# Kernel tuning notes

Hardware: AMD Instinct MI355X
Metric: run time of the kernel (lower is better)

The kernel has to match this reference:

```python
import jax, jax.numpy as jnp
import numpy as np

B, T, D, H, L, E, K, FF, V = 2, 1024, 1024, 16, 3, 8, 2, 4096, 32000
HD = D // H


def _rmsnorm(x):
    return x * jax.lax.rsqrt(jnp.mean(x * x, axis=-1, keepdims=True) + 1e-5)


def _forward(idx, wte, wpe, wq, wk, wv, wo, gate, f1, f2, lm_head):
    Bc, Tc = idx.shape
    x = wte[idx] + wpe[:Tc]            # (B,T,D)
    x = _rmsnorm(x)
    causal = jnp.tril(jnp.ones((Tc, Tc), dtype=bool))
    total_aux = jnp.zeros((), dtype=x.dtype)
    scale = 1.0 / np.sqrt(HD)
    for l in range(L):
        xr = x
        xn = _rmsnorm(x)
        q = (xn @ wq[l].T).reshape(Bc, Tc, H, HD).transpose(0, 2, 1, 3)
        k = (xn @ wk[l].T).reshape(Bc, Tc, H, HD).transpose(0, 2, 1, 3)
        v = (xn @ wv[l].T).reshape(Bc, Tc, H, HD).transpose(0, 2, 1, 3)
        att = jnp.einsum('bhqd,bhkd->bhqk', q, k) * scale
        att = jnp.where(causal, att, -jnp.inf)
        att = jax.nn.softmax(att, axis=-1)
        o = jnp.einsum('bhqk,bhkd->bhqd', att, v)
        o = o.transpose(0, 2, 1, 3).reshape(Bc, Tc, D)
        x = o @ wo[l].T + xr
        # MoE FFN (dense compute over all experts, gather top-k)
        xr = x
        xn = _rmsnorm(x)
        gate_probs = jax.nn.softmax(jnp.einsum('btd,ed->bte', xn, gate[l]), axis=-1)
        topk_vals, topk_idx = jax.lax.top_k(gate_probs, K)   # (B,T,K)
        topk_w = topk_vals / topk_vals.sum(axis=-1, keepdims=True)
        h = jax.nn.relu(jnp.einsum('btd,efd->btef', xn, f1[l]))  # (B,T,E,FF)
        expert_stack = jnp.einsum('btef,edf->bted', h, f2[l])    # (B,T,E,D)
        selected = jnp.take_along_axis(expert_stack, topk_idx[..., None], axis=2)  # (B,T,K,D)
        moe_out = (selected * topk_w[..., None]).sum(axis=2)
        frac = gate_probs.mean(axis=(0, 1))
        total_aux = total_aux + E * jnp.sum(frac * frac)
        x = moe_out + xr
    logits = x @ lm_head.T              # (B,T,V)
    aux_loss = 0.01 * total_aux / L
    return logits, aux_loss


def setup_inputs() -> dict:
    key = jax.random.key(0)
    ks = jax.random.split(key, 12)
    s = 0.02
    return {
        'idx': jax.random.randint(ks[0], (B, T), 0, V, dtype=jnp.int64) if jax.config.jax_enable_x64 else jax.random.randint(ks[0], (B, T), 0, V, dtype=jnp.int32),
        'wte': jax.random.normal(ks[1], (V, D), jnp.float32) * s,
        'wpe': jax.random.normal(ks[2], (T, D), jnp.float32) * s,
        'wq': jax.random.normal(ks[3], (L, D, D), jnp.float32) * s,
        'wk': jax.random.normal(ks[4], (L, D, D), jnp.float32) * s,
        'wv': jax.random.normal(ks[5], (L, D, D), jnp.float32) * s,
        'wo': jax.random.normal(ks[6], (L, D, D), jnp.float32) * s,
        'gate': jax.random.normal(ks[7], (L, E, D), jnp.float32) * s,
        'f1': jax.random.normal(ks[8], (L, E, FF, D), jnp.float32) * s,
        'f2': jax.random.normal(ks[9], (L, E, D, FF), jnp.float32) * s,
        'lm_head': jax.random.normal(ks[10], (V, D), jnp.float32) * s,
    }


def reference(idx, wte, wpe, wq, wk, wv, wo, gate, f1, f2, lm_head):
    return _forward(idx, wte, wpe, wq, wk, wv, wo, gate, f1, f2, lm_head)
```

## Files before the change

### kernel.cpp

```cpp
#include <hip/hip_runtime.h>

typedef unsigned short u16;
typedef __attribute__((ext_vector_type(4))) float f32x4;
typedef __attribute__((ext_vector_type(8))) __bf16 bf16x8;
typedef __attribute__((ext_vector_type(8))) _Float16 f16x8;
typedef __attribute__((ext_vector_type(4))) unsigned short u16x4;
typedef __attribute__((ext_vector_type(8))) unsigned short u16x8;

constexpr int kT = 1024, kD = 1024, kH = 16, kHD = 64, kL = 3, kE = 8;
constexpr int kFF = 4096, kV = 32000, kBT = 2048, kSLOTS = 5120;

__device__ __forceinline__ u16 f2bf(float f) {
  union { float f; unsigned u; } v; v.f = f;
  unsigned r = v.u + 0x7FFFu + ((v.u >> 16) & 1u);
  return (u16)(r >> 16);
}
__device__ __forceinline__ u16 f2h(float x) {
  _Float16 h = (_Float16)x;
  union { _Float16 h; u16 u; } v; v.h = h; return v.u;
}
__device__ __forceinline__ void split2s(float x, u16& h, u16& m) {
  float xs = x * 64.0f;
  _Float16 hh = (_Float16)xs;
  union { _Float16 h; u16 u; } v; v.h = hh; h = v.u;
  float r = xs - (float)hh;
  union { _Float16 h; u16 u; } w; w.h = (_Float16)r; m = w.u;
}

__device__ __forceinline__ void ld_lds16(const void* g, void* l) {
  __builtin_amdgcn_global_load_lds((const __attribute__((address_space(1))) void*)g,
                                   (__attribute__((address_space(3))) void*)l, 16, 0, 0);
}

#define MFMA16(a, b, c) __builtin_amdgcn_mfma_f32_16x16x32_bf16(a, b, c, 0, 0, 0)
#define MFMAH(a, b, c)  __builtin_amdgcn_mfma_f32_16x16x32_f16(a, b, c, 0, 0, 0)

__device__ __forceinline__ float blockReduceSum256(float v) {
  #pragma unroll
  for (int m = 32; m >= 1; m >>= 1) v += __shfl_xor(v, m);
  __shared__ float sh_[4];
  int w = threadIdx.x >> 6;
  if ((threadIdx.x & 63) == 0) sh_[w] = v;
  __syncthreads();
  v = (sh_[0] + sh_[1]) + (sh_[2] + sh_[3]);
  __syncthreads();
  return v;
}


__global__ __launch_bounds__(256) void cast_bf16_k(const float* __restrict__ in,
                                                   u16* __restrict__ out, long n4) {
  long i = (long)blockIdx.x * 256 + threadIdx.x;
  long stride = (long)gridDim.x * 256;
  for (; i < n4; i += stride) {
    f32x4 v = ((const f32x4*)in)[i];
    u16x4 o; o[0] = f2bf(v[0]); o[1] = f2bf(v[1]); o[2] = f2bf(v[2]); o[3] = f2bf(v[3]);
    ((u16x4*)out)[i] = o;
  }
}

__global__ __launch_bounds__(256) void cast_h_k(const float* __restrict__ in,
                                                u16* __restrict__ out, long n4) {
  long i = (long)blockIdx.x * 256 + threadIdx.x;
  long stride = (long)gridDim.x * 256;
  for (; i < n4; i += stride) {
    f32x4 v = ((const f32x4*)in)[i];
    u16x4 o; o[0] = f2h(v[0]); o[1] = f2h(v[1]); o[2] = f2h(v[2]); o[3] = f2h(v[3]);
    ((u16x4*)out)[i] = o;
  }
}

__global__ __launch_bounds__(256) void qkvcomb_k(const float* __restrict__ a,
    const float* __restrict__ b, u16* __restrict__ oP, long plane, long n4) {
  long i = (long)blockIdx.x * 256 + threadIdx.x;
  long stride = (long)gridDim.x * 256;
  for (; i < n4; i += stride) {
    f32x4 v = ((const f32x4*)a)[i] + ((const f32x4*)b)[i];
    u16x4 hh, mm;
    #pragma unroll
    for (int j = 0; j < 4; ++j) {
      u16 h, m; split2s(v[j], h, m);
      hh[j] = h; mm[j] = m;
    }
    ((u16x4*)oP)[i] = hh;
    ((u16x4*)(oP + plane))[i] = mm;
  }
}

__global__ __launch_bounds__(256) void embed_rms_k(const int* __restrict__ idx,
    const float* __restrict__ wte, const float* __restrict__ wpe, float* __restrict__ x) {
  int tok = blockIdx.x, t = threadIdx.x;
  int id = idx[tok];
  int tt = tok & (kT - 1);
  f32x4 a = ((const f32x4*)(wte + (long)id * kD))[t];
  f32x4 p = ((const f32x4*)(wpe + (long)tt * kD))[t];
  f32x4 vv = a + p;
  float ss = vv[0]*vv[0] + vv[1]*vv[1] + vv[2]*vv[2] + vv[3]*vv[3];
  ss = blockReduceSum256(ss);
  float sc = rsqrtf(ss * (1.0f / kD) + 1e-5f);
  vv *= sc;
  ((f32x4*)(x + (long)tok * kD))[t] = vv;
}

__global__ __launch_bounds__(256) void rmsnorm2_k(const float* __restrict__ x,
    float* __restrict__ xnf, u16* __restrict__ xnb) {
  int tok = blockIdx.x, t = threadIdx.x;
  f32x4 vv = ((const f32x4*)(x + (long)tok * kD))[t];
  float ss = blockReduceSum256(vv[0]*vv[0] + vv[1]*vv[1] + vv[2]*vv[2] + vv[3]*vv[3]);
  float sc = rsqrtf(ss * (1.0f / kD) + 1e-5f);
  vv *= sc;
  ((f32x4*)(xnf + (long)tok * kD))[t] = vv;
  u16x4 o;
  o[0] = f2bf(vv[0]); o[1] = f2bf(vv[1]); o[2] = f2bf(vv[2]); o[3] = f2bf(vv[3]);
  ((u16x4*)(xnb + (long)tok * kD))[t] = o;
}

__global__ __launch_bounds__(256) void rmsnorm2h_k(const float* __restrict__ x,
    u16* __restrict__ xnP, long plane) {
  int tok = blockIdx.x, t = threadIdx.x;
  f32x4 vv = ((const f32x4*)(x + (long)tok * kD))[t];
  float ss = blockReduceSum256(vv[0]*vv[0] + vv[1]*vv[1] + vv[2]*vv[2] + vv[3]*vv[3]);
  float sc = rsqrtf(ss * (1.0f / kD) + 1e-5f);
  vv *= sc;
  u16x4 a, b;
  #pragma unroll
  for (int j = 0; j < 4; ++j) {
    u16 h, m; split2s(vv[j], h, m);
    a[j] = h; b[j] = m;
  }
  long o = (long)tok * kD / 4 + t;
  ((u16x4*)xnP)[o] = a;
  ((u16x4*)(xnP + plane))[o] = b;
}

__global__ __launch_bounds__(256) void resid4_rms2h_k(float* __restrict__ x,
    const float* __restrict__ parts, long plane, u16* __restrict__ xnP, long xplane) {
  int tok = blockIdx.x, t = threadIdx.x;
  long o = (long)tok * (kD / 4) + t;
  f32x4 xv = ((f32x4*)x)[o];
  #pragma unroll
  for (int p = 0; p < 4; ++p) xv += ((const f32x4*)(parts + p * plane))[o];
  ((f32x4*)x)[o] = xv;
  float ss = blockReduceSum256(xv[0]*xv[0] + xv[1]*xv[1] + xv[2]*xv[2] + xv[3]*xv[3]);
  float sc = rsqrtf(ss * (1.0f / kD) + 1e-5f);
  f32x4 vv = xv * sc;
  u16x4 a, b;
  #pragma unroll
  for (int j = 0; j < 4; ++j) {
    u16 h, m; split2s(vv[j], h, m);
    a[j] = h; b[j] = m;
  }
  ((u16x4*)xnP)[o] = a;
  ((u16x4*)(xnP + xplane))[o] = b;
}

__global__ __launch_bounds__(256) void moe4_rms2h_k(float* __restrict__ x,
    const float* __restrict__ outsP, long plane, const int* __restrict__ slotOf,
    const float* __restrict__ top2w, u16* __restrict__ xnP, long xplane) {
  int tok = blockIdx.x, t = threadIdx.x;
  int s0 = slotOf[tok*2], s1 = slotOf[tok*2+1];
  float w0 = top2w[tok*2], w1 = top2w[tok*2+1];
  f32x4 a = {0.f,0.f,0.f,0.f}, b = a;
  #pragma unroll
  for (int p = 0; p < 4; ++p) {
    a += ((const f32x4*)(outsP + p * plane + (long)s0 * kD))[t];
    b += ((const f32x4*)(outsP + p * plane + (long)s1 * kD))[t];
  }
  long o = (long)tok * (kD / 4) + t;
  f32x4 xv = ((f32x4*)x)[o];
  xv += a * w0 + b * w1;
  ((f32x4*)x)[o] = xv;
  float ss = blockReduceSum256(xv[0]*xv[0] + xv[1]*xv[1] + xv[2]*xv[2] + xv[3]*xv[3]);
  float sc = rsqrtf(ss * (1.0f / kD) + 1e-5f);
  f32x4 vv = xv * sc;
  u16x4 ha, hb;
  #pragma unroll
  for (int j = 0; j < 4; ++j) {
    u16 h, m; split2s(vv[j], h, m);
    ha[j] = h; hb[j] = m;
  }
  ((u16x4*)xnP)[o] = ha;
  ((u16x4*)(xnP + xplane))[o] = hb;
}

__global__ __launch_bounds__(256) void moe4_cast_h_k(float* __restrict__ x,
    const float* __restrict__ outsP, long plane, const int* __restrict__ slotOf,
    const float* __restrict__ top2w, u16* __restrict__ xn) {
  int tok = blockIdx.x, t = threadIdx.x;
  int s0 = slotOf[tok*2], s1 = slotOf[tok*2+1];
  float w0 = top2w[tok*2], w1 = top2w[tok*2+1];
  f32x4 a = {0.f,0.f,0.f,0.f}, b = a;
  #pragma unroll
  for (int p = 0; p < 4; ++p) {
    a += ((const f32x4*)(outsP + p * plane + (long)s0 * kD))[t];
    b += ((const f32x4*)(outsP + p * plane + (long)s1 * kD))[t];
  }
  long o = (long)tok * (kD / 4) + t;
  f32x4 xv = ((f32x4*)x)[o];
  xv += a * w0 + b * w1;
  u16x4 hv;
  #pragma unroll
  for (int j = 0; j < 4; ++j) hv[j] = f2h(xv[j]);
  ((u16x4*)xn)[o] = hv;
}

__global__ __launch_bounds__(256) void gate_topk_k(const float* __restrict__ x,
    const float* __restrict__ gate_l, float* __restrict__ probs, int* __restrict__ top2e,
    float* __restrict__ top2w, int* __restrict__ counts) {
  int tok = blockIdx.x, t = threadIdx.x;
  f32x4 xv = ((const f32x4*)(x + (long)tok * kD))[t];
  float ss = blockReduceSum256(xv[0]*xv[0] + xv[1]*xv[1] + xv[2]*xv[2] + xv[3]*xv[3]);
  float sc = rsqrtf(ss * (1.0f / kD) + 1e-5f);
  float a[kE];
  #pragma unroll
  for (int e = 0; e < kE; ++e) {
    f32x4 gv = ((const f32x4*)(gate_l + (long)e * kD))[t];
    a[e] = xv[0]*gv[0] + xv[1]*gv[1] + xv[2]*gv[2] + xv[3]*gv[3];
  }
  __shared__ float sh8[kE][4];
  int w = t >> 6, l = t & 63;
  #pragma unroll
  for (int e = 0; e < kE; ++e) {
    float v = a[e];
    #pragma unroll
    for (int m = 32; m >= 1; m >>= 1) v += __shfl_xor(v, m);
    if (l == 0) sh8[e][w] = v;
  }
  __syncthreads();
  if (t == 0) {
    float lg[kE], mx = -1e30f;
    #pragma unroll
    for (int e = 0; e < kE; ++e) {
      lg[e] = (sh8[e][0] + sh8[e][1] + sh8[e][2] + sh8[e][3]) * sc;
      mx = fmaxf(mx, lg[e]);
    }
    float pe[kE], s = 0.f;
    #pragma unroll
    for (int e = 0; e < kE; ++e) { pe[e] = __expf(lg[e] - mx); s += pe[e]; }
    float inv = 1.f / s;
    int i1 = 0;
    #pragma unroll
    for (int e = 1; e < kE; ++e) if (lg[e] > lg[i1]) i1 = e;
    int i2 = (i1 == 0) ? 1 : 0;
    #pragma unroll
    for (int e = 0; e < kE; ++e) if (e != i1 && lg[e] > lg[i2]) i2 = e;
    #pragma unroll
    for (int e = 0; e < kE; ++e) probs[(long)tok * kE + e] = pe[e] * inv;
    float p1 = pe[i1] * inv, p2 = pe[i2] * inv;
    float wn = p1 + p2;
    top2e[tok*2] = i1; top2e[tok*2+1] = i2;
    top2w[tok*2] = p1 / wn; top2w[tok*2+1] = p2 / wn;
    atomicAdd(&counts[i1], 1); atomicAdd(&counts[i2], 1);
  }
}

__global__ void calc_offsets_k(const int* __restrict__ counts, int* __restrict__ offsets) {
  if (threadIdx.x == 0) {
    int o = 0;
    #pragma unroll
    for (int e = 0; e < kE; ++e) { offsets[e] = o; o += (counts[e] + 127) & ~127; }
    offsets[kE] = o;
  }
}

__global__ __launch_bounds__(256) void fill_slots2_k(const int* __restrict__ top2e,
    const int* __restrict__ counts, int* __restrict__ offsets, int* __restrict__ cursors,
    int* __restrict__ rows, int* __restrict__ slotOf) {
  __shared__ int soff[kE + 1];
  if (threadIdx.x == 0) {
    int o = 0;
    #pragma unroll
    for (int e = 0; e < kE; ++e) { soff[e] = o; o += (counts[e] + 127) & ~127; }
    soff[kE] = o;
    if (blockIdx.x == 0) {
      #pragma unroll
      for (int e = 0; e <= kE; ++e) offsets[e] = soff[e];
    }
  }
  __syncthreads();
  int tok = blockIdx.x * 256 + threadIdx.x;
  if (tok >= kBT) return;
  #pragma unroll
  for (int j = 0; j < 2; ++j) {
    int e = top2e[tok*2 + j];
    int pos = atomicAdd(&cursors[e], 1);
    int slot = soff[e] + pos;
    rows[slot] = tok;
    slotOf[tok*2 + j] = slot;
  }
}

__global__ __launch_bounds__(256) void moe_combine4_k(float* __restrict__ x,
    const float* __restrict__ outsP, long plane, const int* __restrict__ slotOf,
    const float* __restrict__ top2w) {
  int tok = blockIdx.x, t = threadIdx.x;
  int s0 = slotOf[tok*2], s1 = slotOf[tok*2+1];
  float w0 = top2w[tok*2], w1 = top2w[tok*2+1];
  f32x4 a = {0.f,0.f,0.f,0.f}, b = a;
  #pragma unroll
  for (int p = 0; p < 4; ++p) {
    a += ((const f32x4*)(outsP + p * plane + (long)s0 * kD))[t];
    b += ((const f32x4*)(outsP + p * plane + (long)s1 * kD))[t];
  }
  f32x4 xv = ((f32x4*)(x + (long)tok * kD))[t];
  xv += a * w0 + b * w1;
  ((f32x4*)(x + (long)tok * kD))[t] = xv;
}

__global__ __launch_bounds__(256) void aux_reduce3_k(const float* __restrict__ probs3,
    long plane, float* __restrict__ outv) {
  int t = threadIdx.x;
  float part[kL][kE] = {};
  for (int i = t; i < kBT; i += 256) {
    #pragma unroll
    for (int l = 0; l < kL; ++l)
      #pragma unroll
      for (int e = 0; e < kE; ++e)
        part[l][e] += probs3[l * plane + (long)i * kE + e];
  }
  __shared__ float sh[kL][kE][4];
  int w = t >> 6, ln = t & 63;
  #pragma unroll
  for (int l = 0; l < kL; ++l)
    #pragma unroll
    for (int e = 0; e < kE; ++e) {
      float v = part[l][e];
      #pragma unroll
      for (int m = 32; m >= 1; m >>= 1) v += __shfl_xor(v, m);
      if (ln == 0) sh[l][e][w] = v;
    }
  __syncthreads();
  if (t == 0) {
    float acc = 0.f;
    #pragma unroll
    for (int l = 0; l < kL; ++l)
      #pragma unroll
      for (int e = 0; e < kE; ++e) {
        float frac = (sh[l][e][0] + sh[l][e][1] + sh[l][e][2] + sh[l][e][3]) * (1.0f / kBT);
        acc += frac * frac;
      }
    outv[0] = 0.01f * (float)kE * acc / (float)kL;
  }
}

__global__ __launch_bounds__(256) void aux_reduce_k(const float* __restrict__ probs,
                                                    float* __restrict__ aux) {
  int t = threadIdx.x;
  float part[kE] = {};
  for (int i = t; i < kBT; i += 256) {
    #pragma unroll
    for (int e = 0; e < kE; ++e) part[e] += probs[(long)i * kE + e];
  }
  __shared__ float sh8[kE][4];
  int w = t >> 6, l = t & 63;
  #pragma unroll
  for (int e = 0; e < kE; ++e) {
    float v = part[e];
    #pragma unroll
    for (int m = 32; m >= 1; m >>= 1) v += __shfl_xor(v, m);
    if (l == 0) sh8[e][w] = v;
  }
  __syncthreads();
  if (t == 0) {
    float acc = 0.f;
    #pragma unroll
    for (int e = 0; e < kE; ++e) {
      float frac = (sh8[e][0] + sh8[e][1] + sh8[e][2] + sh8[e][3]) * (1.0f / kBT);
      acc += frac * frac;
    }
    aux[0] += (float)kE * acc;
  }
}

__global__ void write_aux_k(const float* __restrict__ aux, float* __restrict__ out) {
  if (threadIdx.x == 0) out[0] = 0.01f * aux[0] / (float)kL;
}

enum { P_BF16 = 0, P_BF16_RELU = 1, P_F32 = 2, P_F32_RESID = 3, P_F32_RELU = 4,
       P_SPLIT2_RELU = 5, P_F16_RELU = 6 };

__device__ __forceinline__ int clamp_row(int rv) {
  return ((unsigned)rv < (unsigned)kBT) ? rv : 0;
}

template <bool MPART>
__device__ __forceinline__ void block_mn(int lin, int base, int mArg, int& mb, int& nb) {
  int xcd = lin & 7, c = lin >> 3;
  if (MPART) {
    mb = xcd * mArg + (c % mArg);
    nb = c / mArg;
  } else {
    int swz = xcd * (base >> 3) + c;
    mb = swz % mArg;
    nb = swz / mArg;
  }
}


template <int POST, bool GATHER, bool EXPERT, bool MPART, bool BF32, bool QKV3 = false>
__global__ __launch_bounds__(256) void gemm2h_bt_k(
    const u16* __restrict__ A0, long planeA,
    const void* __restrict__ Bv, const void* __restrict__ Bv1, const void* __restrict__ Bv2,
    long planeB,
    void* __restrict__ C, long planeC,
    const float* __restrict__ resid,
    const int* __restrict__ rows, const int* __restrict__ offsets,
    int N, int K, int lda, long eBstride, int mArg,
    int kParts, int base, long cPart) {
  constexpr int BM = 128, BK = 32;
  int part = blockIdx.x / base;
  int lin = blockIdx.x % base;
  int mb, nb;
  block_mn<MPART>(lin, base, mArg, mb, nb);
  int m0 = mb * BM, n0 = nb * BM;
  const u16* B0 = (const u16*)Bv;
  const float* Bf = (const float*)Bv;
  if (EXPERT) {
    int total = offsets[kE];
    if (m0 >= total) return;
    int e = 0;
    while (offsets[e + 1] <= m0) ++e;
    if (BF32) Bf += (long)e * eBstride; else B0 += (long)e * eBstride;
  }
  __shared__ __align__(16) u16 Ac[BM][64];
  __shared__ __align__(16) u16 Bc[BM][64];
  int t = threadIdx.x;
  int l = t & 63, lr = l & 15, lg = l >> 4;
  int wid = t >> 6;
  int wm = (wid >> 1) * 64, wn = (wid & 1) * 64;

  long asrc[4], bsrc[4];
  int ldst[4];
  #pragma unroll
  for (int it = 0; it < 4; ++it) {
    int d = it * 256 + t;
    int row = d >> 3, pc = d & 7;
    int lc = pc ^ (row & 7);
    int p = lc >> 2, c = lc & 3;
    int grow = GATHER ? clamp_row(rows[m0 + row]) : (m0 + row);
    asrc[it] = (long)p * planeA + (long)grow * lda + c * 8;
    if (!BF32) bsrc[it] = (long)p * planeB + (long)(n0 + row) * K + c * 8;
    ldst[it] = (it * 256 + (t & ~63)) * 8;
  }
  long bsrcF[2];
  int brow[2], bc[2];
  if (BF32) {
    if (QKV3) {
      int ts = n0 >> 10;
      Bf = (ts == 0) ? (const float*)Bv : (ts == 1) ? (const float*)Bv1
                                                    : (const float*)Bv2;
    }
    int nB = QKV3 ? (n0 & 1023) : n0;
    #pragma unroll
    for (int it = 0; it < 2; ++it) {
      int d = it * 256 + t;
      brow[it] = d >> 2; bc[it] = d & 3;
      bsrcF[it] = (long)(nB + brow[it]) * K + bc[it] * 8;
    }
  }
  int sa = lr & 7;
  int cH = (lg ^ sa) * 8;
  int cM = ((4 + lg) ^ sa) * 8;

  f32x4 acc[4][4];
  #pragma unroll
  for (int i = 0; i < 4; ++i)
    #pragma unroll
    for (int j = 0; j < 4; ++j) acc[i][j] = 0.f;

  int kStep = K / kParts;
  int kLo = part * kStep, kHi = kLo + kStep;

  f32x4 pv0[2], pv1[2];
  if (BF32) {
    #pragma unroll
    for (int it = 0; it < 2; ++it) {
      const float* src = Bf + bsrcF[it] + kLo;
      pv0[it] = *(const f32x4*)src;
      pv1[it] = *(const f32x4*)(src + 4);
    }
  }
  for (int k0 = kLo; k0 < kHi; k0 += BK) {
    bool pf = BF32 && (k0 + BK < kHi);
    #pragma unroll
    for (int it = 0; it < 4; ++it) {
      ld_lds16(A0 + asrc[it] + k0, &Ac[0][0] + ldst[it]);
      if (!BF32) ld_lds16(B0 + bsrc[it] + k0, &Bc[0][0] + ldst[it]);
    }
    f32x4 nv0[2], nv1[2];
    if (pf) {
      #pragma unroll
      for (int it = 0; it < 2; ++it) {
        const float* src = Bf + bsrcF[it] + k0 + BK;
        nv0[it] = *(const f32x4*)src;
        nv1[it] = *(const f32x4*)(src + 4);
      }
    }
    if (BF32) {
      #pragma unroll
      for (int it = 0; it < 2; ++it) {
        u16x8 hi, mi;
        #pragma unroll
        for (int j = 0; j < 4; ++j) {
          u16 h, m; split2s(pv0[it][j], h, m); hi[j] = h; mi[j] = m;
        }
        #pragma unroll
        for (int j = 0; j < 4; ++j) {
          u16 h, m; split2s(pv1[it][j], h, m); hi[4 + j] = h; mi[4 + j] = m;
        }
        int r7 = brow[it] & 7;
        *(u16x8*)&Bc[brow[it]][(bc[it] ^ r7) * 8] = hi;
        *(u16x8*)&Bc[brow[it]][((4 + bc[it]) ^ r7) * 8] = mi;
      }
    }
    __syncthreads();
    f16x8 ah[4], am[4];
    #pragma unroll
    for (int i = 0; i < 4; ++i) {
      ah[i] = *(const f16x8*)&Ac[wm + i*16 + lr][cH];
      am[i] = *(const f16x8*)&Ac[wm + i*16 + lr][cM];
    }
    __builtin_amdgcn_s_setprio(1);
    #pragma unroll
    for (int j = 0; j < 4; ++j) {
      f16x8 bh = *(const f16x8*)&Bc[wn + j*16 + lr][cH];
      f16x8 bm = *(const f16x8*)&Bc[wn + j*16 + lr][cM];
      #pragma unroll
      for (int i = 0; i < 4; ++i) {
        acc[i][j] = MFMAH(ah[i], bh, acc[i][j]);
        acc[i][j] = MFMAH(am[i], bh, acc[i][j]);
        acc[i][j] = MFMAH(ah[i], bm, acc[i][j]);
      }
    }
    __builtin_amdgcn_s_setprio(0);
    __syncthreads();
    if (pf) {
      #pragma unroll
      for (int it = 0; it < 2; ++it) { pv0[it] = nv0[it]; pv1[it] = nv1[it]; }
    }
  }
  float* Cf = (float*)C + (long)part * cPart;
  #pragma unroll
  for (int i = 0; i < 4; ++i) {
    #pragma unroll
    for (int r = 0; r < 4; ++r) {
      long m = m0 + wm + i*16 + lg*4 + r;
      #pragma unroll
      for (int j = 0; j < 4; ++j) {
        int n = n0 + wn + j*16 + lr;
        float val = acc[i][j][r] * (1.0f / 4096.0f);
        if (POST == P_F32) {
          Cf[m * N + n] = val;
        } else if (POST == P_F32_RESID) {
          ((float*)C)[m * N + n] = val + resid[m * N + n];
        } else if (POST == P_SPLIT2_RELU) {
          val = fmaxf(val, 0.f);
          u16 h, mm; split2s(val, h, mm);
          u16* Cp = (u16*)C;
          Cp[m * N + n] = h;
          Cp[planeC + m * N + n] = mm;
        }
      }
    }
  }
}


template <int POST, bool GATHER, bool EXPERT, bool BF32>
__global__ __launch_bounds__(512) void gemm2hW_bt_k(
    const u16* __restrict__ A0, long planeA,
    const void* __restrict__ Bv, long planeB,
    void* __restrict__ C, long planeC,
    const int* __restrict__ rows, const int* __restrict__ offsets,
    int N, int K, int lda, long eBstride, int mPerX,
    int kParts, int base, long cPart) {
  constexpr int BM = 128, BN = 256, BK = 32;
  int part = blockIdx.x / base;
  int lin = blockIdx.x % base;
  int xcd = lin & 7, c0 = lin >> 3;
  int m0 = (xcd * mPerX + (c0 % mPerX)) * BM;
  int n0 = (c0 / mPerX) * BN;
  const u16* B0 = (const u16*)Bv;
  const float* Bf = (const float*)Bv;
  if (EXPERT) {
    int total = offsets[kE];
    if (m0 >= total) return;
    int e = 0;
    while (offsets[e + 1] <= m0) ++e;
    if (BF32) Bf += (long)e * eBstride; else B0 += (long)e * eBstride;
  }
  __shared__ __align__(16) u16 Ac[BM][64];
  __shared__ __align__(16) u16 Bc[BN][64];
  int t = threadIdx.x;
  int l = t & 63, lr = l & 15, lg = l >> 4;
  int wid = t >> 6;
  int wm = (wid >> 2) * 64;
  int wn = (wid & 3) * 64;

  long asrc[2], bsrc[4];
  int aldst[2], bldst[4];
  #pragma unroll
  for (int it = 0; it < 2; ++it) {
    int d = it * 512 + t;
    int row = d >> 3, pc = d & 7;
    int lc = pc ^ (row & 7);
    int p = lc >> 2, cc = lc & 3;
    int grow = GATHER ? clamp_row(rows[m0 + row]) : (m0 + row);
    asrc[it] = (long)p * planeA + (long)grow * lda + cc * 8;
    aldst[it] = (it * 512 + (t & ~63)) * 8;
  }
  long bsrcF[2];
  int brow[2], bcc[2];
  if (!BF32) {
    #pragma unroll
    for (int it = 0; it < 4; ++it) {
      int d = it * 512 + t;
      int row = d >> 3, pc = d & 7;
      int lc = pc ^ (row & 7);
      int p = lc >> 2, cc = lc & 3;
      bsrc[it] = (long)p * planeB + (long)(n0 + row) * K + cc * 8;
      bldst[it] = (it * 512 + (t & ~63)) * 8;
    }
  } else {
    #pragma unroll
    for (int it = 0; it < 2; ++it) {
      int d = it * 512 + t;
      brow[it] = d >> 2; bcc[it] = d & 3;
      bsrcF[it] = (long)(n0 + brow[it]) * K + bcc[it] * 8;
    }
  }
  int sa = lr & 7;
  int cH = (lg ^ sa) * 8;
  int cM = ((4 + lg) ^ sa) * 8;

  f32x4 acc[4][4];
  #pragma unroll
  for (int i = 0; i < 4; ++i)
    #pragma unroll
    for (int j = 0; j < 4; ++j) acc[i][j] = 0.f;

  int kStep = K / kParts;
  int kLo = part * kStep, kHi = kLo + kStep;

  f32x4 pv0[2], pv1[2];
  if (BF32) {
    #pragma unroll
    for (int it = 0; it < 2; ++it) {
      const float* src = Bf + bsrcF[it] + kLo;
      pv0[it] = *(const f32x4*)src;
      pv1[it] = *(const f32x4*)(src + 4);
    }
  }
  for (int k0 = kLo; k0 < kHi; k0 += BK) {
    bool pf = BF32 && (k0 + BK < kHi);
    #pragma unroll
    for (int it = 0; it < 2; ++it)
      ld_lds16(A0 + asrc[it] + k0, &Ac[0][0] + aldst[it]);
    if (!BF32) {
      #pragma unroll
      for (int it = 0; it < 4; ++it)
        ld_lds16(B0 + bsrc[it] + k0, &Bc[0][0] + bldst[it]);
    }
    f32x4 nv0[2], nv1[2];
    if (pf) {
      #pragma unroll
      for (int it = 0; it < 2; ++it) {
        const float* src = Bf + bsrcF[it] + k0 + BK;
        nv0[it] = *(const f32x4*)src;
        nv1[it] = *(const f32x4*)(src + 4);
      }
    }
    if (BF32) {
      #pragma unroll
      for (int it = 0; it < 2; ++it) {
        u16x8 hi, mi;
        #pragma unroll
        for (int j = 0; j < 4; ++j) {
          u16 h, m; split2s(pv0[it][j], h, m); hi[j] = h; mi[j] = m;
        }
        #pragma unroll
        for (int j = 0; j < 4; ++j) {
          u16 h, m; split2s(pv1[it][j], h, m); hi[4 + j] = h; mi[4 + j] = m;
        }
        int r7 = brow[it] & 7;
        *(u16x8*)&Bc[brow[it]][(bcc[it] ^ r7) * 8] = hi;
        *(u16x8*)&Bc[brow[it]][((4 + bcc[it]) ^ r7) * 8] = mi;
      }
    }
    __syncthreads();
    f16x8 ah[4], am[4];
    #pragma unroll
    for (int i = 0; i < 4; ++i) {
      ah[i] = *(const f16x8*)&Ac[wm + i*16 + lr][cH];
      am[i] = *(const f16x8*)&Ac[wm + i*16 + lr][cM];
    }
    __builtin_amdgcn_s_setprio(1);
    #pragma unroll
    for (int j = 0; j < 4; ++j) {
      f16x8 bh = *(const f16x8*)&Bc[wn + j*16 + lr][cH];
      f16x8 bm = *(const f16x8*)&Bc[wn + j*16 + lr][cM];
      #pragma unroll
      for (int i = 0; i < 4; ++i) {
        acc[i][j] = MFMAH(ah[i], bh, acc[i][j]);
        acc[i][j] = MFMAH(am[i], bh, acc[i][j]);
        acc[i][j] = MFMAH(ah[i], bm, acc[i][j]);
      }
    }
    __builtin_amdgcn_s_setprio(0);
    __syncthreads();
    if (pf) {
      #pragma unroll
      for (int it = 0; it < 2; ++it) { pv0[it] = nv0[it]; pv1[it] = nv1[it]; }
    }
  }
  float* Cf = (float*)C + (long)part * cPart;
  #pragma unroll
  for (int i = 0; i < 4; ++i) {
    #pragma unroll
    for (int r = 0; r < 4; ++r) {
      long m = m0 + wm + i*16 + lg*4 + r;
      #pragma unroll
      for (int j = 0; j < 4; ++j) {
        int n = n0 + wn + j*16 + lr;
        float val = acc[i][j][r] * (1.0f / 4096.0f);
        if (POST == P_F32) {
          Cf[m * N + n] = val;
        } else if (POST == P_SPLIT2_RELU) {
          val = fmaxf(val, 0.f);
          u16 h, mm; split2s(val, h, mm);
          u16* Cp = (u16*)C;
          Cp[m * N + n] = h;
          Cp[planeC + m * N + n] = mm;
        }
      }
    }
  }
}


template <int POST, bool EXPERT, bool GATHER, bool HALF, bool BCONV, bool MPART>
__global__ __launch_bounds__(256) void gemm_bt_k(
    const u16* __restrict__ A, const void* __restrict__ Bv, void* __restrict__ C,
    const int* __restrict__ rows, const int* __restrict__ offsets,
    int N, int K, int lda, long eBstride, float oscale, int mArg,
    int kParts, int base, long cPart) {
  constexpr int BM = 128, BK = 64;
  int part = blockIdx.x / base;
  int lin = blockIdx.x % base;
  int mb, nb;
  block_mn<MPART>(lin, base, mArg, mb, nb);
  int m0 = mb * BM, n0 = nb * BM;
  const float* Bf = (const float*)Bv;
  const u16*   Bh = (const u16*)Bv;
  if (EXPERT) {
    int total = offsets[kE];
    if (m0 >= total) return;
    int e = 0;
    while (offsets[e + 1] <= m0) ++e;
    if (BCONV) Bf += (long)e * eBstride; else Bh += (long)e * eBstride;
  }
  __shared__ __align__(16) u16 As[BM][BK];
  __shared__ __align__(16) u16 Bs[BM][BK];
  int t = threadIdx.x;
  int l = t & 63, lr = l & 15, lg = l >> 4;
  int wid = t >> 6;
  int wm = (wid >> 1) * 64, wn = (wid & 1) * 64;

  long asrc[4], bsrc[4];
  int ldst[4];
  #pragma unroll
  for (int it = 0; it < 4; ++it) {
    int d = it * 256 + t;
    int row = d >> 3, pc = d & 7;
    int c = pc ^ (row & 7);
    int grow = GATHER ? clamp_row(rows[m0 + row]) : (m0 + row);
    asrc[it] = (long)grow * lda + c * 8;
    if (!BCONV) bsrc[it] = (long)(n0 + row) * K + c * 8;
    ldst[it] = (it * 256 + (t & ~63)) * 8;
  }
  long bsrcC[4];
  int bdst[4];
  if (BCONV) {
    #pragma unroll
    for (int it = 0; it < 4; ++it) {
      int d = it * 256 + t;
      int row = d >> 3, lc = d & 7;
      bsrcC[it] = (long)(n0 + row) * K + lc * 8;
      bdst[it] = row * BK + (lc ^ (row & 7)) * 8;
    }
  }
  f32x4 acc[4][4];
  #pragma unroll
  for (int i = 0; i < 4; ++i)
    #pragma unroll
    for (int j = 0; j < 4; ++j) acc[i][j] = 0.f;

  int kStep = K / kParts;
  int kLo = part * kStep, kHi = kLo + kStep;
  for (int k0 = kLo; k0 < kHi; k0 += BK) {
    #pragma unroll
    for (int it = 0; it < 4; ++it)
      ld_lds16(A + asrc[it] + k0, &As[0][0] + ldst[it]);
    if (!BCONV) {
      #pragma unroll
      for (int it = 0; it < 4; ++it)
        ld_lds16(Bh + bsrc[it] + k0, &Bs[0][0] + ldst[it]);
    } else {
      #pragma unroll
      for (int it = 0; it < 4; ++it) {
        const float* src = Bf + bsrcC[it] + k0;
        f32x4 v0 = *(const f32x4*)src;
        f32x4 v1 = *(const f32x4*)(src + 4);
        u16x8 o;
        #pragma unroll
        for (int j = 0; j < 4; ++j) {
          o[j] = HALF ? f2h(v0[j]) : f2bf(v0[j]);
          o[4 + j] = HALF ? f2h(v1[j]) : f2bf(v1[j]);
        }
        *(u16x8*)(&Bs[0][0] + bdst[it]) = o;
      }
    }
    __syncthreads();
    __builtin_amdgcn_s_setprio(1);
    #pragma unroll
    for (int kk = 0; kk < 2; ++kk) {
      int ca = ((kk * 4 + lg) ^ (lr & 7)) * 8;
      #pragma unroll
      for (int i = 0; i < 4; ++i)
        #pragma unroll
        for (int j = 0; j < 4; ++j) {
          if (HALF) {
            f16x8 af = *(const f16x8*)&As[wm + i*16 + lr][ca];
            f16x8 bq = *(const f16x8*)&Bs[wn + j*16 + lr][ca];
            acc[i][j] = MFMAH(af, bq, acc[i][j]);
          } else {
            bf16x8 af = *(const bf16x8*)&As[wm + i*16 + lr][ca];
            bf16x8 bq = *(const bf16x8*)&Bs[wn + j*16 + lr][ca];
            acc[i][j] = MFMA16(af, bq, acc[i][j]);
          }
        }
    }
    __builtin_amdgcn_s_setprio(0);
    __syncthreads();
  }
  #pragma unroll
  for (int i = 0; i < 4; ++i) {
    #pragma unroll
    for (int r = 0; r < 4; ++r) {
      long m = m0 + wm + i*16 + lg*4 + r;
      #pragma unroll
      for (int j = 0; j < 4; ++j) {
        int n = n0 + wn + j*16 + lr;
        float val = acc[i][j][r] * oscale;
        if (POST == P_BF16_RELU)       ((u16*)C)[m * N + n] = f2bf(fmaxf(val, 0.f));
        else if (POST == P_F16_RELU)   ((u16*)C)[m * N + n] = f2h(fmaxf(val, 0.f));
        else if (POST == P_F32)        ((float*)C + (long)part * cPart)[m * N + n] = val;
      }
    }
  }
}


template <int POST, bool GATHER, bool EXPERT>
__global__ __launch_bounds__(256) void sgemm_bt_k(
    const float* __restrict__ A, const float* __restrict__ B, float* __restrict__ C,
    const float* __restrict__ resid, const int* __restrict__ rows,
    const int* __restrict__ offsets, int N, int K, int lda, long eBstride) {
  constexpr int BM = 128, BN = 128, BK = 32;
  int m0 = blockIdx.x * BM, n0 = blockIdx.y * BN;
  if (EXPERT) {
    int total = offsets[kE];
    if (m0 >= total) return;
    int e = 0;
    while (offsets[e + 1] <= m0) ++e;
    B += (long)e * eBstride;
  }
  __shared__ float Ast[BK][BM];
  __shared__ float Bst[BK][BN];
  int t = threadIdx.x, tx = t & 15, ty = t >> 4;
  long asrc[4], bsrc[4];
  #pragma unroll
  for (int it = 0; it < 4; ++it) {
    int c = it * 256 + t;
    int row = c >> 3, kc = (c & 7) * 4;
    int gr = GATHER ? clamp_row(rows[m0 + row]) : (m0 + row);
    asrc[it] = (long)gr * lda + kc;
    bsrc[it] = (long)(n0 + row) * K + kc;
  }
  f32x4 accv[8][2];
  #pragma unroll
  for (int i = 0; i < 8; ++i) { accv[i][0] = 0.f; accv[i][1] = 0.f; }

  for (int k0 = 0; k0 < K; k0 += BK) {
    #pragma unroll
    for (int it = 0; it < 4; ++it) {
      int c = it * 256 + t;
      int row = c >> 3, kc = (c & 7) * 4;
      f32x4 av = *(const f32x4*)(A + asrc[it] + k0);
      f32x4 bv = *(const f32x4*)(B + bsrc[it] + k0);
      #pragma unroll
      for (int j = 0; j < 4; ++j) { Ast[kc + j][row] = av[j]; Bst[kc + j][row] = bv[j]; }
    }
    __syncthreads();
    #pragma unroll
    for (int kk = 0; kk < BK; ++kk) {
      f32x4 a0 = *(const f32x4*)&Ast[kk][ty * 4];
      f32x4 a1 = *(const f32x4*)&Ast[kk][64 + ty * 4];
      f32x4 b0 = *(const f32x4*)&Bst[kk][tx * 4];
      f32x4 b1 = *(const f32x4*)&Bst[kk][64 + tx * 4];
      float as[8] = {a0[0], a0[1], a0[2], a0[3], a1[0], a1[1], a1[2], a1[3]};
      #pragma unroll
      for (int i = 0; i < 8; ++i) {
        accv[i][0] += b0 * as[i];
        accv[i][1] += b1 * as[i];
      }
    }
    __syncthreads();
  }
  #pragma unroll
  for (int ih = 0; ih < 2; ++ih)
    #pragma unroll
    for (int i = 0; i < 4; ++i) {
      long m = m0 + ih * 64 + ty * 4 + i;
      #pragma unroll
      for (int jh = 0; jh < 2; ++jh) {
        long n = n0 + jh * 64 + tx * 4;
        f32x4 val = accv[ih * 4 + i][jh];
        if (POST == P_F32_RELU) {
          #pragma unroll
          for (int j = 0; j < 4; ++j) val[j] = fmaxf(val[j], 0.f);
        }
        if (POST == P_F32_RESID) val += *(const f32x4*)&resid[m * N + n];
        *(f32x4*)&C[m * N + n] = val;
      }
    }
}


__global__ __launch_bounds__(256) void attn2h_k(
    const u16* __restrict__ qkvP, long qplane,
    u16* __restrict__ oP, long oplane) {
  int qt = (int)gridDim.x - 1 - (int)blockIdx.x;
  int bh = blockIdx.y;
  int b = bh >> 4, h = bh & 15;
  const int ldq = 3 * kD;
  long hbq = (long)b * kT * ldq + h * kHD;
  long hbo = (long)b * kT * kD + h * kHD;
  int t = threadIdx.x, w = t >> 6, l = t & 63;
  int lr = l & 15, lg = l >> 4;

  __shared__ __align__(16) u16 Ks[2][64][72];
  __shared__ __align__(16) u16 Vt[2][64][72];
  __shared__ __align__(16) u16 Ps[2][4][16][72];

  f16x8 qf0[2], qf1[2];
  {
    long qrow = qt * 64 + w * 16 + lr;
    const u16* qp = qkvP + hbq + qrow * ldq;
    #pragma unroll
    for (int kc = 0; kc < 2; ++kc) {
      qf0[kc] = *(const f16x8*)(qp + kc * 32 + lg * 8);
      qf1[kc] = *(const f16x8*)(qp + qplane + kc * 32 + lg * 8);
    }
  }
  int qg = qt * 64 + w * 16 + lg * 4;

  float mrow[4], lsum[4];
  f32x4 accO[4];
  #pragma unroll
  for (int r = 0; r < 4; ++r) { mrow[r] = -1e30f; lsum[r] = 0.f; }
  #pragma unroll
  for (int j = 0; j < 4; ++j) accO[j] = 0.f;

  for (int it = 0; it <= qt; ++it) {
    #pragma unroll
    for (int p = 0; p < 2; ++p) {
      #pragma unroll
      for (int s = 0; s < 2; ++s) {
        int c = s * 256 + t;
        int row = c >> 3, col = (c & 7) * 8;
        long gi = (long)p * qplane + hbq + (long)(it * 64 + row) * ldq + col;
        *(u16x8*)&Ks[p][row][col] = *(const u16x8*)(qkvP + kD + gi);
        u16x8 vv = *(const u16x8*)(qkvP + 2 * kD + gi);
        #pragma unroll
        for (int j = 0; j < 8; ++j) Vt[p][col + j][row] = vv[j];
      }
    }
    __syncthreads();

    f32x4 s4[4];
    __builtin_amdgcn_s_setprio(1);
    #pragma unroll
    for (int j = 0; j < 4; ++j) {
      f32x4 z = {0.f, 0.f, 0.f, 0.f};
      #pragma unroll
      for (int kc = 0; kc < 2; ++kc) {
        f16x8 kh = *(const f16x8*)&Ks[0][j*16 + lr][kc*32 + lg*8];
        f16x8 km = *(const f16x8*)&Ks[1][j*16 + lr][kc*32 + lg*8];
        z = MFMAH(qf0[kc], kh, z);
        z = MFMAH(qf1[kc], kh, z);
        z = MFMAH(qf0[kc], km, z);
      }
      s4[j] = z;
    }
    __builtin_amdgcn_s_setprio(0);
    #pragma unroll
    for (int j = 0; j < 4; ++j)
      #pragma unroll
      for (int r = 0; r < 4; ++r) {
        float sv = s4[j][r] * (0.125f / 4096.0f);
        if (it * 64 + j * 16 + lr > qg + r) sv = -1e30f;
        s4[j][r] = sv;
      }
    float alpha[4];
    #pragma unroll
    for (int r = 0; r < 4; ++r) {
      float mx = fmaxf(fmaxf(s4[0][r], s4[1][r]), fmaxf(s4[2][r], s4[3][r]));
      mx = fmaxf(mx, __shfl_xor(mx, 1));
      mx = fmaxf(mx, __shfl_xor(mx, 2));
      mx = fmaxf(mx, __shfl_xor(mx, 4));
      mx = fmaxf(mx, __shfl_xor(mx, 8));
      float mi = fmaxf(mrow[r], mx);
      alpha[r] = __expf(mrow[r] - mi);
      mrow[r] = mi;
    }
    float rs[4] = {0.f, 0.f, 0.f, 0.f};
    #pragma unroll
    for (int j = 0; j < 4; ++j)
      #pragma unroll
      for (int r = 0; r < 4; ++r) {
        float p = __expf(s4[j][r] - mrow[r]);
        rs[r] += p;
        u16 hh, mm; split2s(p, hh, mm);
        Ps[0][w][lg*4 + r][j*16 + lr] = hh;
        Ps[1][w][lg*4 + r][j*16 + lr] = mm;
      }
    #pragma unroll
    for (int r = 0; r < 4; ++r) {
      float x2 = rs[r];
      x2 += __shfl_xor(x2, 1);
      x2 += __shfl_xor(x2, 2);
      x2 += __shfl_xor(x2, 4);
      x2 += __shfl_xor(x2, 8);
      lsum[r] = lsum[r] * alpha[r] + x2;
    }
    #pragma unroll
    for (int j = 0; j < 4; ++j)
      #pragma unroll
      for (int r = 0; r < 4; ++r) accO[j][r] *= alpha[r];
    __syncthreads();

    f16x8 ph[2], pm[2];
    #pragma unroll
    for (int kc = 0; kc < 2; ++kc) {
      ph[kc] = *(const f16x8*)&Ps[0][w][lr][kc*32 + lg*8];
      pm[kc] = *(const f16x8*)&Ps[1][w][lr][kc*32 + lg*8];
    }
    __builtin_amdgcn_s_setprio(1);
    #pragma unroll
    for (int j2 = 0; j2 < 4; ++j2) {
      #pragma unroll
      for (int kc = 0; kc < 2; ++kc) {
        f16x8 vh = *(const f16x8*)&Vt[0][j2*16 + lr][kc*32 + lg*8];
        f16x8 vm = *(const f16x8*)&Vt[1][j2*16 + lr][kc*32 + lg*8];
        accO[j2] = MFMAH(ph[kc], vh, accO[j2]);
        accO[j2] = MFMAH(pm[kc], vh, accO[j2]);
        accO[j2] = MFMAH(ph[kc], vm, accO[j2]);
      }
    }
    __builtin_amdgcn_s_setprio(0);
    __syncthreads();
  }
  #pragma unroll
  for (int j2 = 0; j2 < 4; ++j2)
    #pragma unroll
    for (int r = 0; r < 4; ++r) {
      float ov = accO[j2][r] * (1.0f / 4096.0f) / lsum[r];
      long row = qt * 64 + w * 16 + lg * 4 + r;
      long idx = hbo + row * kD + j2 * 16 + lr;
      u16 hh, mm; split2s(ov, hh, mm);
      oP[idx] = hh;
      oP[oplane + idx] = mm;
    }
}


__global__ __launch_bounds__(256) void attn_f32_k(
    const float* __restrict__ qkv, float* __restrict__ of32, int ldq) {
  int qt = blockIdx.x;
  int bh = blockIdx.y;
  int b = bh >> 4, h = bh & 15;
  long hbq = (long)b * kT * ldq + h * kHD;
  long hbo = (long)b * kT * kD + h * kHD;
  int t = threadIdx.x, qr = t >> 2, sub = t & 3;

  __shared__ float Qs[64][68], Ks[64][68], Vs[64][68], Ps[64][68];

  const float* q = qkv;
  const float* k = qkv + kD;
  const float* v = qkv + 2 * kD;

  #pragma unroll
  for (int it = 0; it < 4; ++it) {
    int c = it * 256 + t, row = c >> 4, c4 = (c & 15) * 4;
    f32x4 qv = *(const f32x4*)(q + hbq + (long)(qt * 64 + row) * ldq + c4);
    #pragma unroll
    for (int j = 0; j < 4; ++j) Qs[row][c4 + j] = qv[j];
  }
  __syncthreads();
  f32x4 qreg[16];
  #pragma unroll
  for (int d4 = 0; d4 < 16; ++d4) qreg[d4] = *(const f32x4*)&Qs[qr][d4 * 4];
  int qg = qt * 64 + qr;

  float mrow = -1e30f, lsum = 0.f;
  f32x4 accO[4];
  #pragma unroll
  for (int i = 0; i < 4; ++i) accO[i] = 0.f;

  for (int itl = 0; itl <= qt; ++itl) {
    #pragma unroll
    for (int it = 0; it < 4; ++it) {
      int c = it * 256 + t, row = c >> 4, c4 = (c & 15) * 4;
      long gi = hbq + (long)(itl * 64 + row) * ldq + c4;
      f32x4 kv = *(const f32x4*)(k + gi);
      f32x4 vv = *(const f32x4*)(v + gi);
      #pragma unroll
      for (int j = 0; j < 4; ++j) { Ks[row][c4 + j] = kv[j]; Vs[row][c4 + j] = vv[j]; }
    }
    __syncthreads();

    float s[16];
    #pragma unroll
    for (int kk = 0; kk < 16; ++kk) {
      int key = kk * 4 + sub;
      f32x4 a = {0.f, 0.f, 0.f, 0.f};
      #pragma unroll
      for (int d4 = 0; d4 < 16; ++d4) a += qreg[d4] * *(const f32x4*)&Ks[key][d4 * 4];
      float sv = (a[0] + a[1] + a[2] + a[3]) * 0.125f;
      if (itl * 64 + key > qg) sv = -1e30f;
      s[kk] = sv;
    }
    float mx = s[0];
    #pragma unroll
    for (int kk = 1; kk < 16; ++kk) mx = fmaxf(mx, s[kk]);
    mx = fmaxf(mx, __shfl_xor(mx, 1));
    mx = fmaxf(mx, __shfl_xor(mx, 2));
    float mi = fmaxf(mrow, mx);
    float alpha = __expf(mrow - mi);
    mrow = mi;
    float rs = 0.f;
    #pragma unroll
    for (int kk = 0; kk < 16; ++kk) {
      float p = __expf(s[kk] - mi);
      rs += p;
      Ps[qr][kk * 4 + sub] = p;
    }
    rs += __shfl_xor(rs, 1);
    rs += __shfl_xor(rs, 2);
    lsum = lsum * alpha + rs;
    #pragma unroll
    for (int i = 0; i < 4; ++i) accO[i] *= alpha;
    #pragma unroll
    for (int key2 = 0; key2 < 64; ++key2) {
      float p = Ps[qr][key2];
      #pragma unroll
      for (int i4 = 0; i4 < 4; ++i4)
        accO[i4] += p * *(const f32x4*)&Vs[key2][sub * 16 + i4 * 4];
    }
    __syncthreads();
  }
  float inv = 1.f / lsum;
  #pragma unroll
  for (int i4 = 0; i4 < 4; ++i4) {
    f32x4 ov = accO[i4] * inv;
    *(f32x4*)(of32 + hbo + (long)qg * kD + sub * 16 + i4 * 4) = ov;
  }
}


extern "C" void kernel_launch(void* const* d_in, const int* in_sizes, int n_in,
                              void* d_out, int out_size, void* d_ws, size_t ws_size,
                              hipStream_t stream) {
  const int*   idx  = (const int*)  d_in[0];
  const float* wte  = (const float*)d_in[1];
  const float* wpe  = (const float*)d_in[2];
  const float* wq   = (const float*)d_in[3];
  const float* wk   = (const float*)d_in[4];
  const float* wv   = (const float*)d_in[5];
  const float* wo   = (const float*)d_in[6];
  const float* gate = (const float*)d_in[7];
  const float* f1   = (const float*)d_in[8];
  const float* f2   = (const float*)d_in[9];
  const float* lmh  = (const float*)d_in[10];
  float* out = (float*)d_out;

  char* ws = (char*)d_ws;
  size_t off = 0;
  auto alloc = [&](size_t b) -> char* {
    char* p = ws + off;
    off += (b + 255) & ~(size_t)255;
    return p;
  };

  constexpr long PLN_XN = (long)kBT * kD;
  constexpr long PLN_Q3 = (long)kBT * 3 * kD;
  constexpr long PLN_FF = (long)kE * kFF * kD;
  constexpr long PLN_H = (long)kSLOTS * kFF;
  constexpr long PLN_OUTS = (long)kSLOTS * kD;
  constexpr long PLN_PR = (long)kBT * kE;

  float* x     = (float*)alloc((size_t)kBT * kD * 4);
  float* outs  = (float*)alloc((size_t)4 * PLN_OUTS * 4);
  float* probs3= (float*)alloc((size_t)kL * PLN_PR * 4);
  int*   top2e = (int*)  alloc((size_t)kBT * 2 * 4);
  float* top2w = (float*)alloc((size_t)kBT * 2 * 4);
  int*   meta  = (int*)  alloc(64 * 4);
  int* counts = meta; int* cursors = meta + 8; int* offs = meta + 16;
  int*   rows  = (int*)  alloc((size_t)kSLOTS * 4);
  int*   slotOf= (int*)  alloc((size_t)kBT * 2 * 4);
  float* aux   = (float*)alloc(256);
  size_t off_shared = off;

  u16*   xnP   = (u16*)  alloc((size_t)2 * PLN_XN * 2);
  float* qkvf  = (float*)alloc((size_t)PLN_Q3 * 4);
  u16*   qkvP  = (u16*)  alloc((size_t)2 * PLN_Q3 * 2);
  u16*   ofP   = (u16*)  alloc((size_t)2 * PLN_XN * 2);
  u16*   hP    = (u16*)  alloc((size_t)2 * PLN_H * 2);
  u16*   lmb   = (u16*)  alloc((size_t)kV * kD * 2);
  bool fast = (off <= ws_size);
  float* qkvp1 = (float*)hP;

  dim3 gAttn(kT / 64, 2 * kH);
  int bQKV = (kBT / 128) * (3 * kD / 128);
  int bWO  = (kBT / 128) * (kD / 128);
  int nF1W = (kSLOTS / 128) * (kFF / 256);
  int bF2  = (kSLOTS / 128) * (kD / 128);
  int nF1s = (kSLOTS / 128) * (kFF / 128);
  int nLM  = (kBT / 128) * (kV / 128);

  if (fast) {
    cast_h_k<<<4096, 256, 0, stream>>>(lmh, lmb, (long)kV * kD / 4);
    embed_rms_k<<<kBT, 256, 0, stream>>>(idx, wte, wpe, x);
    rmsnorm2h_k<<<kBT, 256, 0, stream>>>(x, xnP, PLN_XN);

    for (int li = 0; li < kL; ++li) {
      size_t dd = (size_t)li * kD * kD;
      gemm2h_bt_k<P_F32, false, false, true, true, true><<<2 * bQKV, 256, 0, stream>>>(
          xnP, PLN_XN, wq + dd, wk + dd, wv + dd, 0,
          qkvf, 0, nullptr, nullptr, nullptr, 3 * kD, kD, kD, 0, 2,
          2, bQKV, (long)(qkvp1 - qkvf));
      qkvcomb_k<<<2048, 256, 0, stream>>>(qkvf, qkvp1, qkvP, PLN_Q3, PLN_Q3 / 4);
      attn2h_k<<<gAttn, 256, 0, stream>>>(qkvP, PLN_Q3, ofP, PLN_XN);
      gemm2h_bt_k<P_F32, false, false, true, true><<<4 * bWO, 256, 0, stream>>>(
          ofP, PLN_XN, wo + dd, nullptr, nullptr, 0,
          outs, 0, nullptr, nullptr, nullptr, kD, kD, kD, 0, 2,
          4, bWO, PLN_OUTS);
      resid4_rms2h_k<<<kBT, 256, 0, stream>>>(x, outs, PLN_OUTS, xnP, PLN_XN);
      hipMemsetAsync(meta, 0, 64, stream);
      gate_topk_k<<<kBT, 256, 0, stream>>>(x, gate + (size_t)li * kE * kD,
                                           probs3 + (size_t)li * PLN_PR,
                                           top2e, top2w, counts);
      fill_slots2_k<<<kBT / 256, 256, 0, stream>>>(top2e, counts, offs, cursors,
                                                   rows, slotOf);
      size_t fd = (size_t)li * PLN_FF;
      if (li < 2) {
        gemm2hW_bt_k<P_SPLIT2_RELU, true, true, true><<<nF1W, 512, 0, stream>>>(
            xnP, PLN_XN, f1 + fd, 0, hP, PLN_H, rows, offs,
            kFF, kD, kD, (long)kFF * kD, kSLOTS / 128 / 8,
            1, nF1W, 0);
        gemm2h_bt_k<P_F32, false, true, true, true><<<4 * bF2, 256, 0, stream>>>(
            hP, PLN_H, f2 + fd, nullptr, nullptr, 0, outs, 0, nullptr, nullptr, offs,
            kD, kFF, kFF, (long)kD * kFF, kSLOTS / 128 / 8,
            4, bF2, PLN_OUTS);
        moe4_rms2h_k<<<kBT, 256, 0, stream>>>(x, outs, PLN_OUTS, slotOf, top2w,
                                              xnP, PLN_XN);
      } else {
        gemm_bt_k<P_F16_RELU, true, true, true, true, true><<<nF1s, 256, 0, stream>>>(
            xnP, f1 + fd, hP, rows, offs, kFF, kD, kD, (long)kFF * kD,
            1.0f / 64.0f, kSLOTS / 128 / 8, 1, nF1s, 0);
        gemm_bt_k<P_F32, true, false, true, true, true><<<4 * bF2, 256, 0, stream>>>(
            hP, f2 + fd, outs, nullptr, offs, kD, kFF, kFF, (long)kD * kFF,
            1.0f, kSLOTS / 128 / 8, 4, bF2, PLN_OUTS);
        moe4_cast_h_k<<<kBT, 256, 0, stream>>>(x, outs, PLN_OUTS, slotOf, top2w, xnP);
      }
    }
    gemm_bt_k<P_F32, false, false, true, false, false><<<nLM, 256, 0, stream>>>(
        xnP, lmb, out, nullptr, nullptr, kV, kD, kD, 0, 1.0f, kBT / 128,
        1, nLM, 0);
    aux_reduce3_k<<<1, 256, 0, stream>>>(probs3, PLN_PR, out + (size_t)kBT * kV);
    return;
  }

  off = off_shared;
  float* xnf   = (float*)alloc((size_t)kBT * kD * 4);
  u16*   xnb   = (u16*)  alloc((size_t)kBT * kD * 2);
  float* qkvf32= (float*)alloc((size_t)kBT * 3 * kD * 4);
  float* off32 = (float*)alloc((size_t)kBT * kD * 4);
  float* hbuf  = (float*)alloc((size_t)kSLOTS * kFF * 4);
  u16* hbuf16 = (u16*)hbuf;

  hipMemsetAsync(aux, 0, 4, stream);
  embed_rms_k<<<kBT, 256, 0, stream>>>(idx, wte, wpe, x);
  dim3 gF1s(kSLOTS / 128, kFF / 128);
  dim3 gF2s(kSLOTS / 128, kD / 128);
  for (int li = 0; li < kL; ++li) {
    size_t dd = (size_t)li * kD * kD;
    rmsnorm2_k<<<kBT, 256, 0, stream>>>(x, xnf, xnb);
    dim3 gP(kBT / 128, kD / 128);
    sgemm_bt_k<P_F32, false, false><<<gP, 256, 0, stream>>>(
        xnf, wq + dd, qkvf32, nullptr, nullptr, nullptr, 3 * kD, kD, kD, 0);
    sgemm_bt_k<P_F32, false, false><<<gP, 256, 0, stream>>>(
        xnf, wk + dd, qkvf32 + kD, nullptr, nullptr, nullptr, 3 * kD, kD, kD, 0);
    sgemm_bt_k<P_F32, false, false><<<gP, 256, 0, stream>>>(
        xnf, wv + dd, qkvf32 + 2 * kD, nullptr, nullptr, nullptr, 3 * kD, kD, kD, 0);
    attn_f32_k<<<gAttn, 256, 0, stream>>>(qkvf32, off32, 3 * kD);
    sgemm_bt_k<P_F32_RESID, false, false><<<gP, 256, 0, stream>>>(
        off32, wo + dd, x, x, nullptr, nullptr, kD, kD, kD, 0);
    rmsnorm2_k<<<kBT, 256, 0, stream>>>(x, xnf, xnb);
    hipMemsetAsync(meta, 0, 64, stream);
    gate_topk_k<<<kBT, 256, 0, stream>>>(x, gate + (size_t)li * kE * kD,
                                         probs3, top2e, top2w, counts);
    calc_offsets_k<<<1, 64, 0, stream>>>(counts, offs);
    fill_slots2_k<<<kBT / 256, 256, 0, stream>>>(top2e, counts, offs, cursors,
                                                 rows, slotOf);
    size_t fd = (size_t)li * kE * kFF * kD;
    if (li < 2) {
      sgemm_bt_k<P_F32_RELU, true, true><<<gF1s, 256, 0, stream>>>(
          xnf, f1 + fd, hbuf, nullptr, rows, offs, kFF, kD, kD, (long)kFF * kD);
      sgemm_bt_k<P_F32, false, true><<<gF2s, 256, 0, stream>>>(
          hbuf, f2 + fd, outs, nullptr, nullptr, offs, kD, kFF, kFF, (long)kD * kFF);
    } else {
      gemm_bt_k<P_BF16_RELU, true, true, false, true, false><<<nF1s, 256, 0, stream>>>(
          xnb, f1 + fd, hbuf16, rows, offs, kFF, kD, kD, (long)kFF * kD,
          1.0f, kSLOTS / 128, 1, nF1s, 0);
      gemm_bt_k<P_F32, true, false, false, true, false><<<bF2, 256, 0, stream>>>(
          hbuf16, f2 + fd, outs, nullptr, offs, kD, kFF, kFF, (long)kD * kFF,
          1.0f, kSLOTS / 128, 1, bF2, 0);
    }
    hipMemsetAsync(outs + PLN_OUTS, 0, 3 * PLN_OUTS * 4, stream);
    moe_combine4_k<<<kBT, 256, 0, stream>>>(x, outs, PLN_OUTS, slotOf, top2w);
    aux_reduce_k<<<1, 256, 0, stream>>>(probs3, aux);
  }
  cast_bf16_k<<<2048, 256, 0, stream>>>(x, xnb, (long)kBT * kD / 4);
  gemm_bt_k<P_F32, false, false, false, true, false><<<nLM, 256, 0, stream>>>(
      xnb, lmh, out, nullptr, nullptr, kV, kD, kD, 0, 1.0f, kBT / 128,
      1, nLM, 0);
  write_aux_k<<<1, 64, 0, stream>>>(aux, out + (size_t)kBT * kV);
}
```

Baseline: 1.842 ms.

## Fuse lm_head fp16 cast into GEMM B-load and prefetch converted B tiles

Drops the standalone kernel that casts the 32000x1024 lm_head to fp16 and instead has the LM-head GEMM read fp32 weights and convert them on the fly (BCONV path). It also adds register double-buffering for the BCONV path, loading the next K-tile's fp32 B values while the current tile is converted and multiplied. This removes a full write-and-reread of the converted weight matrix, but the GEMM now reads twice the bytes for B and carries extra registers for the prefetch.

```diff
diff --git a/kernel.cpp b/kernel.cpp
--- a/kernel.cpp
+++ b/kernel.cpp
@@ -55,17 +55,6 @@
   for (; i < n4; i += stride) {
     f32x4 v = ((const f32x4*)in)[i];
     u16x4 o; o[0] = f2bf(v[0]); o[1] = f2bf(v[1]); o[2] = f2bf(v[2]); o[3] = f2bf(v[3]);
-    ((u16x4*)out)[i] = o;
-  }
-}
-
-__global__ __launch_bounds__(256) void cast_h_k(const float* __restrict__ in,
-                                                u16* __restrict__ out, long n4) {
-  long i = (long)blockIdx.x * 256 + threadIdx.x;
-  long stride = (long)gridDim.x * 256;
-  for (; i < n4; i += stride) {
-    f32x4 v = ((const f32x4*)in)[i];
-    u16x4 o; o[0] = f2h(v[0]); o[1] = f2h(v[1]); o[2] = f2h(v[2]); o[3] = f2h(v[3]);
     ((u16x4*)out)[i] = o;
   }
 }
@@ -797,7 +786,18 @@
 
   int kStep = K / kParts;
   int kLo = part * kStep, kHi = kLo + kStep;
+
+  f32x4 pv0[4], pv1[4];
+  if (BCONV) {
+    #pragma unroll
+    for (int it = 0; it < 4; ++it) {
+      const float* src = Bf + bsrcC[it] + kLo;
+      pv0[it] = *(const f32x4*)src;
+      pv1[it] = *(const f32x4*)(src + 4);
+    }
+  }
   for (int k0 = kLo; k0 < kHi; k0 += BK) {
+    bool pf = BCONV && (k0 + BK < kHi);
     #pragma unroll
     for (int it = 0; it < 4; ++it)
       ld_lds16(A + asrc[it] + k0, &As[0][0] + ldst[it]);
@@ -805,17 +805,24 @@
       #pragma unroll
       for (int it = 0; it < 4; ++it)
         ld_lds16(Bh + bsrc[it] + k0, &Bs[0][0] + ldst[it]);
-    } else {
+    }
+    f32x4 nv0[4], nv1[4];
+    if (pf) {
       #pragma unroll
       for (int it = 0; it < 4; ++it) {
-        const float* src = Bf + bsrcC[it] + k0;
-        f32x4 v0 = *(const f32x4*)src;
-        f32x4 v1 = *(const f32x4*)(src + 4);
+        const float* src = Bf + bsrcC[it] + k0 + BK;
+        nv0[it] = *(const f32x4*)src;
+        nv1[it] = *(const f32x4*)(src + 4);
+      }
+    }
+    if (BCONV) {
+      #pragma unroll
+      for (int it = 0; it < 4; ++it) {
         u16x8 o;
         #pragma unroll
         for (int j = 0; j < 4; ++j) {
-          o[j] = HALF ? f2h(v0[j]) : f2bf(v0[j]);
-          o[4 + j] = HALF ? f2h(v1[j]) : f2bf(v1[j]);
+          o[j] = HALF ? f2h(pv0[it][j]) : f2bf(pv0[it][j]);
+          o[4 + j] = HALF ? f2h(pv1[it][j]) : f2bf(pv1[it][j]);
         }
         *(u16x8*)(&Bs[0][0] + bdst[it]) = o;
       }
@@ -842,6 +849,10 @@
     }
     __builtin_amdgcn_s_setprio(0);
     __syncthreads();
+    if (pf) {
+      #pragma unroll
+      for (int it = 0; it < 4; ++it) { pv0[it] = nv0[it]; pv1[it] = nv1[it]; }
+    }
   }
   #pragma unroll
   for (int i = 0; i < 4; ++i) {
@@ -1227,7 +1238,6 @@
   u16*   qkvP  = (u16*)  alloc((size_t)2 * PLN_Q3 * 2);
   u16*   ofP   = (u16*)  alloc((size_t)2 * PLN_XN * 2);
   u16*   hP    = (u16*)  alloc((size_t)2 * PLN_H * 2);
-  u16*   lmb   = (u16*)  alloc((size_t)kV * kD * 2);
   bool fast = (off <= ws_size);
   float* qkvp1 = (float*)hP;
 
@@ -1240,7 +1250,6 @@
   int nLM  = (kBT / 128) * (kV / 128);
 
   if (fast) {
-    cast_h_k<<<4096, 256, 0, stream>>>(lmh, lmb, (long)kV * kD / 4);
     embed_rms_k<<<kBT, 256, 0, stream>>>(idx, wte, wpe, x);
     rmsnorm2h_k<<<kBT, 256, 0, stream>>>(x, xnP, PLN_XN);
 
@@ -1285,8 +1294,8 @@
         moe4_cast_h_k<<<kBT, 256, 0, stream>>>(x, outs, PLN_OUTS, slotOf, top2w, xnP);
       }
     }
-    gemm_bt_k<P_F32, false, false, true, false, false><<<nLM, 256, 0, stream>>>(
-        xnP, lmb, out, nullptr, nullptr, kV, kD, kD, 0, 1.0f, kBT / 128,
+    gemm_bt_k<P_F32, false, false, true, true, false><<<nLM, 256, 0, stream>>>(
+        xnP, lmh, out, nullptr, nullptr, kV, kD, kD, 0, 1.0f, kBT / 128,
         1, nLM, 0);
     aux_reduce3_k<<<1, 256, 0, stream>>>(probs3, PLN_PR, out + (size_t)kBT * kV);
     return;
```

Measured after the change: 1.784 ms. 1.03x faster.
